# Kernel tuning notes

Measured on AMD Instinct MI355X. Metric: run time of the kernel, lower is better.

The kernel has to match this reference:

```python
import jax, jax.numpy as jnp
import numpy as np
from jax import lax

DIM = 384
NE = 8
TOPK = 2
HID = 4 * DIM
N, H, W = 32, 32, 32
EPS = 1e-6


def setup_inputs() -> dict:
    key = jax.random.key(0)
    ks = jax.random.split(key, 12)
    s = 0.02
    return {
        "input": jax.random.normal(ks[0], (N, DIM, H, W), dtype=jnp.float32),
        "dw_w": jax.random.normal(ks[1], (DIM, 1, 7, 7), dtype=jnp.float32) * s,
        "dw_b": jnp.zeros((DIM,), dtype=jnp.float32),
        "ln_g": jnp.ones((DIM,), dtype=jnp.float32),
        "ln_b": jnp.zeros((DIM,), dtype=jnp.float32),
        "gate_w": jax.random.normal(ks[2], (NE, DIM), dtype=jnp.float32) * s,
        "w1": jax.random.normal(ks[3], (NE, DIM, HID), dtype=jnp.float32) * s,
        "b1": jnp.zeros((NE, HID), dtype=jnp.float32),
        "w2": jax.random.normal(ks[4], (NE, HID, DIM), dtype=jnp.float32) * s,
        "b2": jnp.zeros((NE, DIM), dtype=jnp.float32),
        "layer_scale": jnp.ones((DIM, 1, 1), dtype=jnp.float32) * 1e-6,
    }


def reference(input, dw_w, dw_b, ln_g, ln_b, gate_w, w1, b1, w2, b2, layer_scale):
    # depthwise 7x7 conv, padding 3, groups=DIM  (NCHW)
    x = lax.conv_general_dilated(
        input, dw_w, window_strides=(1, 1), padding=((3, 3), (3, 3)),
        dimension_numbers=("NCHW", "OIHW", "NCHW"), feature_group_count=DIM,
    ) + dw_b[None, :, None, None]
    # permute to NHWC, layernorm over C with eps=1e-6
    x = jnp.transpose(x, (0, 2, 3, 1))
    mu = jnp.mean(x, axis=-1, keepdims=True)
    var = jnp.mean(jnp.square(x - mu), axis=-1, keepdims=True)
    x = (x - mu) * lax.rsqrt(var + EPS) * ln_g + ln_b

    x_flat = x.reshape(-1, DIM)  # [T, C]
    logits = x_flat @ gate_w.T   # [T, NE]
    topv, topi = lax.top_k(logits, TOPK)
    weights = jax.nn.softmax(topv, axis=-1)  # [T, K]

    # combine: out[t] = sum_e gate_e[t] * Expert_e(x_flat[t]), gate nonzero only for top-k
    out = jnp.zeros_like(x_flat)
    for e in range(NE):
        we = jnp.sum(jnp.where(topi == e, weights, 0.0), axis=-1)  # [T]
        h = jax.nn.gelu(x_flat @ w1[e] + b1[e], approximate=False)
        y = h @ w2[e] + b2[e]
        out = out + y * we[:, None]

    out = out.reshape(N, H, W, DIM)
    out = jnp.transpose(out, (0, 3, 1, 2))  # back to NCHW
    out = layer_scale[None] * out           # [C,1,1] broadcast
    # stochastic_depth prob 0.0 -> identity
    return input + out
```

## Files before the change

### kernel.cpp

```cpp
#include <hip/hip_runtime.h>
#include <hip/hip_bf16.h>

typedef __attribute__((ext_vector_type(4))) float  f32x4;
typedef __attribute__((ext_vector_type(8))) short  s16x8;
typedef __attribute__((ext_vector_type(8))) unsigned short u16x8;
typedef __attribute__((ext_vector_type(4))) unsigned short u16x4;

#define DIM 384
#define NE 8
#define HID 1536
#define NB 32
#define HW 1024
#define T_TOK 32768

__device__ __forceinline__ unsigned short f2bf(float f) {
    unsigned int u = __float_as_uint(f);
    u = (u + 0x7fffu + ((u >> 16) & 1u)) >> 16;
    return (unsigned short)u;
}
__device__ __forceinline__ float bf2f(unsigned short u) {
    return __uint_as_float((unsigned int)u << 16);
}

__global__ __launch_bounds__(256) void k_transpose(const float* __restrict__ src,
                                                   unsigned short* __restrict__ dst,
                                                   int R, int C) {
    int b = blockIdx.x;
    int ctiles = C >> 5;
    int rtiles = R >> 5;
    int ct = b % ctiles;
    int rt = (b / ctiles) % rtiles;
    int e  = b / (ctiles * rtiles);
    __shared__ float t[32][33];
    int tid = threadIdx.x;
    const float* s = src + (size_t)e * R * C;
    unsigned short* d = dst + (size_t)e * C * R;
#pragma unroll
    for (int k = 0; k < 4; ++k) {
        int idx = k * 256 + tid;
        int rr = idx >> 5, cc = idx & 31;
        t[rr][cc] = s[(size_t)(rt * 32 + rr) * C + ct * 32 + cc];
    }
    __syncthreads();
#pragma unroll
    for (int k = 0; k < 4; ++k) {
        int idx = k * 256 + tid;
        int cc = idx >> 5, rr = idx & 31;
        d[(size_t)(ct * 32 + cc) * R + rt * 32 + rr] = f2bf(t[rr][cc]);
    }
}

__global__ __launch_bounds__(256) void k_conv(const float* __restrict__ in,
                                              const float* __restrict__ dw_w,
                                              const float* __restrict__ dw_b,
                                              float* __restrict__ xconv) {
    int nc = blockIdx.x;
    int c = nc % DIM;
    __shared__ float tile[38 * 38];
    __shared__ float wt[49];
    const float* plane = in + (size_t)nc * HW;
    int tid = threadIdx.x;
    if (tid < 49) wt[tid] = dw_w[c * 49 + tid];
    for (int idx = tid; idx < 38 * 38; idx += 256) {
        int ty = idx / 38, tx = idx % 38;
        int ih = ty - 3, iw = tx - 3;
        float v = 0.f;
        if ((unsigned)ih < 32u && (unsigned)iw < 32u) v = plane[ih * 32 + iw];
        tile[idx] = v;
    }
    __syncthreads();
    float bias = dw_b[c];
    int w = tid & 31, h0 = (tid >> 5) << 2;
    float acc[4] = {bias, bias, bias, bias};
#pragma unroll
    for (int iy = 0; iy < 10; ++iy) {
        float r[7];
#pragma unroll
        for (int dx = 0; dx < 7; ++dx) r[dx] = tile[(h0 + iy) * 38 + w + dx];
#pragma unroll
        for (int o = 0; o < 4; ++o) {
            int dy = iy - o;
            if (dy >= 0 && dy < 7) {
                float a = 0.f;
#pragma unroll
                for (int dx = 0; dx < 7; ++dx) a += r[dx] * wt[dy * 7 + dx];
                acc[o] += a;
            }
        }
    }
    float* outp = xconv + (size_t)nc * HW;
#pragma unroll
    for (int o = 0; o < 4; ++o) outp[(h0 + o) * 32 + w] = acc[o];
}

__global__ __launch_bounds__(256) void k_ln_gate(const float* __restrict__ xconv,
                                                 const float* __restrict__ ln_g,
                                                 const float* __restrict__ ln_b,
                                                 const float* __restrict__ gate_w,
                                                 unsigned short* __restrict__ lnout,
                                                 int* __restrict__ lists,
                                                 float* __restrict__ wgts,
                                                 int* __restrict__ counts) {
    __shared__ float xs[32][385];
    __shared__ float gw[8][384];
    __shared__ float gls[384], bls[384];
    __shared__ int hcnt[8], hbase[8];
    __shared__ int lexp[32][2];
    __shared__ int lpos[32][2];
    __shared__ float lw[32][2];

    int b = blockIdx.x;
    int n = b >> 5;
    int hw0 = (b & 31) << 5;
    int tid = threadIdx.x;

    for (int i = tid; i < 384; i += 256) { gls[i] = ln_g[i]; bls[i] = ln_b[i]; }
    for (int i = tid; i < 8 * 384; i += 256) gw[i / 384][i % 384] = gate_w[i];
    if (tid < 8) hcnt[tid] = 0;

    const float* base = xconv + (size_t)n * DIM * HW + hw0;
#pragma unroll
    for (int k = 0; k < 48; ++k) {
        int idx = k * 256 + tid;
        int c = idx >> 5, j = idx & 31;
        xs[j][c] = base[(size_t)c * HW + j];
    }
    __syncthreads();

    int tok = tid >> 3, jj = tid & 7;
    float sum = 0.f, sq = 0.f;
#pragma unroll
    for (int k = 0; k < 48; ++k) {
        float v = xs[tok][jj + 8 * k];
        sum += v; sq += v * v;
    }
#pragma unroll
    for (int m = 1; m < 8; m <<= 1) { sum += __shfl_xor(sum, m); sq += __shfl_xor(sq, m); }
    float mu = sum * (1.f / 384.f);
    float var = sq * (1.f / 384.f) - mu * mu;
    float rstd = rsqrtf(var + 1e-6f);

    int tglob = n * HW + hw0 + tok;
    float p[8] = {0, 0, 0, 0, 0, 0, 0, 0};
#pragma unroll
    for (int k = 0; k < 48; ++k) {
        int c = jj + 8 * k;
        float v = (xs[tok][c] - mu) * rstd * gls[c] + bls[c];
        lnout[(size_t)tglob * DIM + c] = f2bf(v);
#pragma unroll
        for (int e = 0; e < 8; ++e) p[e] += v * gw[e][c];
    }
#pragma unroll
    for (int e = 0; e < 8; ++e)
#pragma unroll
        for (int m = 1; m < 8; m <<= 1) p[e] += __shfl_xor(p[e], m);

    if (jj == 0) {
        int i0 = 0; float v0 = p[0];
#pragma unroll
        for (int e = 1; e < 8; ++e) if (p[e] > v0) { v0 = p[e]; i0 = e; }
        int i1 = -1; float v1 = -1e30f;
#pragma unroll
        for (int e = 0; e < 8; ++e) if (e != i0 && p[e] > v1) { v1 = p[e]; i1 = e; }
        float w0 = 1.f / (1.f + __expf(v1 - v0));
        float w1 = 1.f - w0;
        lexp[tok][0] = i0; lexp[tok][1] = i1;
        lw[tok][0] = w0;  lw[tok][1] = w1;
        lpos[tok][0] = atomicAdd(&hcnt[i0], 1);
        lpos[tok][1] = atomicAdd(&hcnt[i1], 1);
    }
    __syncthreads();
    if (tid < 8) hbase[tid] = atomicAdd(&counts[tid], hcnt[tid]);
    __syncthreads();
    if (jj == 0) {
#pragma unroll
        for (int s = 0; s < 2; ++s) {
            int e = lexp[tok][s];
            int pos = hbase[e] + lpos[tok][s];
            lists[e * T_TOK + pos] = (tglob << 1) | s;
            wgts[e * T_TOK + pos] = lw[tok][s];
        }
    }
}

__global__ __launch_bounds__(512, 2) void k_moe(const unsigned short* __restrict__ ln,
                                                const unsigned short* __restrict__ w1t,
                                                const unsigned short* __restrict__ w2t,
                                                const float* __restrict__ b1,
                                                const float* __restrict__ b2,
                                                const int* __restrict__ lists,
                                                const float* __restrict__ wgts,
                                                const int* __restrict__ counts,
                                                unsigned short* __restrict__ y0,
                                                unsigned short* __restrict__ y1) {
    int e    = blockIdx.x & 7;
    int tile = blockIdx.x >> 3;
    int cnt = counts[e];
    if (tile * 128 >= cnt) return;

    __shared__ unsigned short X[128][392];
    __shared__ unsigned short Hs[128][136];
    __shared__ int   ents[128];
    __shared__ float wrow[128];

    int tid = threadIdx.x;
    if (tid < 128) {
        int idx = tile * 128 + tid;
        if (idx < cnt) { ents[tid] = lists[e * T_TOK + idx]; wrow[tid] = wgts[e * T_TOK + idx]; }
        else           { ents[tid] = -1;                     wrow[tid] = 0.f; }
    }
    __syncthreads();

    {
        int row = tid >> 2, q = tid & 3;
        int ent = ents[row];
        int tok = (ent < 0) ? 0 : (ent >> 1);
        const u16x8* src = (const u16x8*)(ln + (size_t)tok * DIM);
        u16x8* dst = (u16x8*)(&X[row][0]);
#pragma unroll
        for (int r = 0; r < 12; ++r) dst[q + r * 4] = __builtin_nontemporal_load(&src[q + r * 4]);
    }
    __syncthreads();

    int wid = tid >> 6;
    int lane = tid & 63;
    int lr = lane & 15;
    int lq = lane >> 4;

    const s16x8* q1 = (const s16x8*)(w1t + ((size_t)e * HID + wid * 16 + lr) * DIM + lq * 8);
    const s16x8* q2 = (const s16x8*)(w2t + ((size_t)e * DIM + wid * 48 + lr) * HID + lq * 8);

    f32x4 Yacc[3][8] = {};

    for (int hc = 0; hc < 12; ++hc) {
        const s16x8* q1h = q1 + hc * 6144;
        s16x8 wall[12];
#pragma unroll
        for (int k = 0; k < 12; ++k) wall[k] = q1h[k * 4];
        f32x4 bv = *(const f32x4*)&b1[e * HID + hc * 128 + wid * 16 + lq * 4];
        f32x4 Hf[8];
#pragma unroll
        for (int m = 0; m < 8; ++m) Hf[m] = bv;
        __builtin_amdgcn_s_setprio(1);
#pragma unroll
        for (int k = 0; k < 12; ++k) {
#pragma unroll
            for (int m = 0; m < 8; ++m) {
                s16x8 a = *(const s16x8*)&X[m * 16 + lr][k * 32 + lq * 8];
                Hf[m] = __builtin_amdgcn_mfma_f32_16x16x32_bf16(wall[k], a, Hf[m], 0, 0, 0);
            }
        }
        __builtin_amdgcn_s_setprio(0);
        s16x8 vall[12];
#pragma unroll
        for (int t = 0; t < 12; ++t) {
            int nj = t % 3, k2 = t / 3;
            vall[t] = q2[nj * 3072 + hc * 16 + k2 * 4];
        }
#pragma unroll
        for (int m = 0; m < 8; ++m) {
            u16x4 pk;
#pragma unroll
            for (int r = 0; r < 4; ++r) {
                float v = Hf[m][r];
                float t = v * fmaf(v * v, -0.07135481627f, -1.5957691216f);
                float g = v * __builtin_amdgcn_rcpf(1.f + __expf(t));
                pk[r] = f2bf(g);
            }
            *(u16x4*)&Hs[m * 16 + lr][wid * 16 + lq * 4] = pk;
        }
        asm volatile("s_waitcnt lgkmcnt(0)" ::: "memory");
        __builtin_amdgcn_s_barrier();
        __builtin_amdgcn_sched_barrier(0);
        __builtin_amdgcn_s_setprio(1);
#pragma unroll
        for (int k2 = 0; k2 < 4; ++k2) {
#pragma unroll
            for (int m = 0; m < 8; ++m) {
                s16x8 a = *(const s16x8*)&Hs[m * 16 + lr][k2 * 32 + lq * 8];
#pragma unroll
                for (int nj = 0; nj < 3; ++nj) {
                    Yacc[nj][m] = __builtin_amdgcn_mfma_f32_16x16x32_bf16(vall[k2 * 3 + nj], a, Yacc[nj][m], 0, 0, 0);
                }
            }
        }
        __builtin_amdgcn_s_setprio(0);
        asm volatile("s_waitcnt lgkmcnt(0)" ::: "memory");
        __builtin_amdgcn_s_barrier();
        __builtin_amdgcn_sched_barrier(0);
    }

    f32x4 b2v[3];
#pragma unroll
    for (int nj = 0; nj < 3; ++nj)
        b2v[nj] = *(const f32x4*)&b2[e * DIM + wid * 48 + nj * 16 + lq * 4];
#pragma unroll
    for (int m = 0; m < 8; ++m) {
        int row = m * 16 + lr;
        int ent = ents[row];
        if (ent >= 0) {
            float wv = wrow[row];
            int tok = ent >> 1;
            unsigned short* yb = (ent & 1) ? y1 : y0;
#pragma unroll
            for (int nj = 0; nj < 3; ++nj) {
                u16x4 pk;
#pragma unroll
                for (int r = 0; r < 4; ++r)
                    pk[r] = f2bf((Yacc[nj][m][r] + b2v[nj][r]) * wv);
                *(u16x4*)(yb + (size_t)tok * DIM + wid * 48 + nj * 16 + lq * 4) = pk;
            }
        }
    }
}

__global__ __launch_bounds__(256) void k_final(const float* __restrict__ input,
                                               const float* __restrict__ ls,
                                               const unsigned short* __restrict__ y0,
                                               const unsigned short* __restrict__ y1,
                                               float* __restrict__ out) {
    int b = blockIdx.x;
    int ct = b % 12;
    int hwt = (b / 12) % 32;
    int n = b / (12 * 32);
    int c0 = ct * 32, hw0 = hwt * 32;
    __shared__ float t[32][33];
    int tid = threadIdx.x;
    int t0 = n * HW + hw0;
#pragma unroll
    for (int k = 0; k < 2; ++k) {
        int idx = k * 256 + tid;
        int tl = idx >> 4, pr = idx & 15;
        size_t o = (size_t)(t0 + tl) * DIM + c0 + pr * 2;
        unsigned int a = *(const unsigned int*)(y0 + o);
        unsigned int c = *(const unsigned int*)(y1 + o);
        t[tl][pr * 2]     = bf2f((unsigned short)a) + bf2f((unsigned short)c);
        t[tl][pr * 2 + 1] = bf2f((unsigned short)(a >> 16)) + bf2f((unsigned short)(c >> 16));
    }
    __syncthreads();
#pragma unroll
    for (int k = 0; k < 4; ++k) {
        int idx = k * 256 + tid;
        int cl = idx >> 5, j = idx & 31;
        size_t o = ((size_t)n * DIM + c0 + cl) * HW + hw0 + j;
        out[o] = input[o] + ls[c0 + cl] * t[j][cl];
    }
}

extern "C" void kernel_launch(void* const* d_in, const int* in_sizes, int n_in,
                              void* d_out, int out_size, void* d_ws, size_t ws_size,
                              hipStream_t stream) {
    const float* input  = (const float*)d_in[0];
    const float* dw_w   = (const float*)d_in[1];
    const float* dw_b   = (const float*)d_in[2];
    const float* ln_g   = (const float*)d_in[3];
    const float* ln_b   = (const float*)d_in[4];
    const float* gate_w = (const float*)d_in[5];
    const float* w1     = (const float*)d_in[6];
    const float* b1     = (const float*)d_in[7];
    const float* w2     = (const float*)d_in[8];
    const float* b2     = (const float*)d_in[9];
    const float* lscale = (const float*)d_in[10];

    const size_t SZ_PLANE = (size_t)NB * DIM * HW * 4;
    const size_t SZ_YBF   = (size_t)T_TOK * DIM * 2;
    char* ws = (char*)d_ws;
    float* xconv = (float*)(ws + 0);
    unsigned short* y0 = (unsigned short*)(ws + 0);
    unsigned short* y1 = (unsigned short*)(ws + SZ_YBF);
    unsigned short* lnb = (unsigned short*)(ws + SZ_PLANE);
    unsigned short* w1t = (unsigned short*)(ws + SZ_PLANE + 25165824);
    unsigned short* w2t = (unsigned short*)(ws + SZ_PLANE + 25165824 + 9437184);
    int*   lists  = (int*)(ws + SZ_PLANE + 25165824 + 2 * 9437184);
    float* wgt    = (float*)(ws + SZ_PLANE + 25165824 + 2 * 9437184 + 1048576);
    int*   counts = (int*)(ws + SZ_PLANE + 25165824 + 2 * 9437184 + 2 * 1048576);
    const size_t needed = SZ_PLANE + 25165824 + 2 * 9437184 + 2 * 1048576 + 256;
    if (ws_size < needed) return;

    hipMemsetAsync(counts, 0, 32, stream);
    k_transpose<<<8 * 12 * 48, 256, 0, stream>>>(w1, w1t, DIM, HID);
    k_transpose<<<8 * 48 * 12, 256, 0, stream>>>(w2, w2t, HID, DIM);
    k_conv<<<NB * DIM, 256, 0, stream>>>(input, dw_w, dw_b, xconv);
    k_ln_gate<<<T_TOK / 32, 256, 0, stream>>>(xconv, ln_g, ln_b, gate_w, lnb, lists, wgt, counts);
    k_moe<<<NE * 256, 512, 0, stream>>>(lnb, w1t, w2t, b1, b2, lists, wgt, counts, y0, y1);
    k_final<<<NB * 32 * 12, 256, 0, stream>>>(input, lscale, y0, y1, (float*)d_out);
}
```

Baseline: 427.6 us.

## Switch MoE expert GEMMs and activations from bf16 to fp8 e4m3

Weights, layernorm output and the GELU hidden activations are now stored as fp8 e4m3 rather than bf16, and both expert matmuls use the fp8 16x16x32 MFMA. The aim is to halve global and LDS traffic for weights and tokens. The next hidden chunk's w1 fragment is now loaded after the first GEMM so it overlaps the GELU and second GEMM, and w2 loads are issued earlier. The instruction shape keeps K=32, so MFMA issue count is unchanged. It also costs noticeably more quantization error, which is masked only by the tiny layer_scale.

```diff
diff --git a/kernel.cpp b/kernel.cpp
--- a/kernel.cpp
+++ b/kernel.cpp
@@ -1,10 +1,11 @@
 #include <hip/hip_runtime.h>
 #include <hip/hip_bf16.h>
+#include <hip/hip_fp8.h>
 
 typedef __attribute__((ext_vector_type(4))) float  f32x4;
-typedef __attribute__((ext_vector_type(8))) short  s16x8;
 typedef __attribute__((ext_vector_type(8))) unsigned short u16x8;
 typedef __attribute__((ext_vector_type(4))) unsigned short u16x4;
+typedef long long f8x8;
 
 #define DIM 384
 #define NE 8
@@ -21,10 +22,14 @@
 __device__ __forceinline__ float bf2f(unsigned short u) {
     return __uint_as_float((unsigned int)u << 16);
 }
-
-__global__ __launch_bounds__(256) void k_transpose(const float* __restrict__ src,
-                                                   unsigned short* __restrict__ dst,
-                                                   int R, int C) {
+__device__ __forceinline__ unsigned char f2fp8(float f) {
+    __hip_fp8_e4m3 h(f);
+    return (unsigned char)h.__x;
+}
+
+__global__ __launch_bounds__(256) void k_transpose8(const float* __restrict__ src,
+                                                    unsigned char* __restrict__ dst,
+                                                    int R, int C) {
     int b = blockIdx.x;
     int ctiles = C >> 5;
     int rtiles = R >> 5;
@@ -34,7 +39,7 @@
     __shared__ float t[32][33];
     int tid = threadIdx.x;
     const float* s = src + (size_t)e * R * C;
-    unsigned short* d = dst + (size_t)e * C * R;
+    unsigned char* d = dst + (size_t)e * C * R;
 #pragma unroll
     for (int k = 0; k < 4; ++k) {
         int idx = k * 256 + tid;
@@ -42,12 +47,12 @@
         t[rr][cc] = s[(size_t)(rt * 32 + rr) * C + ct * 32 + cc];
     }
     __syncthreads();
-#pragma unroll
-    for (int k = 0; k < 4; ++k) {
-        int idx = k * 256 + tid;
-        int cc = idx >> 5, rr = idx & 31;
-        d[(size_t)(ct * 32 + cc) * R + rt * 32 + rr] = f2bf(t[rr][cc]);
-    }
+    int cc = tid >> 3, r4 = tid & 7;
+    unsigned int pk = 0;
+#pragma unroll
+    for (int i = 0; i < 4; ++i)
+        pk |= (unsigned int)f2fp8(t[r4 * 4 + i][cc]) << (8 * i);
+    *(unsigned int*)&d[(size_t)(ct * 32 + cc) * R + rt * 32 + r4 * 4] = pk;
 }
 
 __global__ __launch_bounds__(256) void k_conv(const float* __restrict__ in,
@@ -97,7 +102,7 @@
                                                  const float* __restrict__ ln_g,
                                                  const float* __restrict__ ln_b,
                                                  const float* __restrict__ gate_w,
-                                                 unsigned short* __restrict__ lnout,
+                                                 unsigned char* __restrict__ lnout,
                                                  int* __restrict__ lists,
                                                  float* __restrict__ wgts,
                                                  int* __restrict__ counts) {
@@ -146,7 +151,7 @@
     for (int k = 0; k < 48; ++k) {
         int c = jj + 8 * k;
         float v = (xs[tok][c] - mu) * rstd * gls[c] + bls[c];
-        lnout[(size_t)tglob * DIM + c] = f2bf(v);
+        lnout[(size_t)tglob * DIM + c] = f2fp8(v);
 #pragma unroll
         for (int e = 0; e < 8; ++e) p[e] += v * gw[e][c];
     }
@@ -183,9 +188,9 @@
     }
 }
 
-__global__ __launch_bounds__(512, 2) void k_moe(const unsigned short* __restrict__ ln,
-                                                const unsigned short* __restrict__ w1t,
-                                                const unsigned short* __restrict__ w2t,
+__global__ __launch_bounds__(512, 2) void k_moe(const unsigned char* __restrict__ ln,
+                                                const unsigned char* __restrict__ w1t,
+                                                const unsigned char* __restrict__ w2t,
                                                 const float* __restrict__ b1,
                                                 const float* __restrict__ b2,
                                                 const int* __restrict__ lists,
@@ -198,8 +203,8 @@
     int cnt = counts[e];
     if (tile * 128 >= cnt) return;
 
-    __shared__ unsigned short X[128][392];
-    __shared__ unsigned short Hs[128][136];
+    __shared__ unsigned char X[128][400];
+    __shared__ unsigned char Hs[128][136];
     __shared__ int   ents[128];
     __shared__ float wrow[128];
 
@@ -216,9 +221,9 @@
         int ent = ents[row];
         int tok = (ent < 0) ? 0 : (ent >> 1);
         const u16x8* src = (const u16x8*)(ln + (size_t)tok * DIM);
-        u16x8* dst = (u16x8*)(&X[row][0]);
-#pragma unroll
-        for (int r = 0; r < 12; ++r) dst[q + r * 4] = __builtin_nontemporal_load(&src[q + r * 4]);
+#pragma unroll
+        for (int r = 0; r < 6; ++r)
+            *(u16x8*)&X[row][(q + r * 4) * 16] = __builtin_nontemporal_load(&src[q + r * 4]);
     }
     __syncthreads();
 
@@ -227,16 +232,22 @@
     int lr = lane & 15;
     int lq = lane >> 4;
 
-    const s16x8* q1 = (const s16x8*)(w1t + ((size_t)e * HID + wid * 16 + lr) * DIM + lq * 8);
-    const s16x8* q2 = (const s16x8*)(w2t + ((size_t)e * DIM + wid * 48 + lr) * HID + lq * 8);
+    const unsigned char* pw1 = w1t + ((size_t)e * HID + wid * 16 + lr) * DIM + lq * 8;
+    const unsigned char* pw2 = w2t + ((size_t)e * DIM + wid * 48 + lr) * HID + lq * 8;
 
     f32x4 Yacc[3][8] = {};
 
+    f8x8 wall[12];
+#pragma unroll
+    for (int k = 0; k < 12; ++k) wall[k] = *(const f8x8*)(pw1 + k * 32);
+
     for (int hc = 0; hc < 12; ++hc) {
-        const s16x8* q1h = q1 + hc * 6144;
-        s16x8 wall[12];
-#pragma unroll
-        for (int k = 0; k < 12; ++k) wall[k] = q1h[k * 4];
+        f8x8 vall[12];
+#pragma unroll
+        for (int t = 0; t < 12; ++t) {
+            int nj = t % 3, k2 = t / 3;
+            vall[t] = *(const f8x8*)(pw2 + (size_t)nj * 16 * HID + hc * 128 + k2 * 32);
+        }
         f32x4 bv = *(const f32x4*)&b1[e * HID + hc * 128 + wid * 16 + lq * 4];
         f32x4 Hf[8];
 #pragma unroll
@@ -246,28 +257,27 @@
         for (int k = 0; k < 12; ++k) {
 #pragma unroll
             for (int m = 0; m < 8; ++m) {
-                s16x8 a = *(const s16x8*)&X[m * 16 + lr][k * 32 + lq * 8];
-                Hf[m] = __builtin_amdgcn_mfma_f32_16x16x32_bf16(wall[k], a, Hf[m], 0, 0, 0);
+                f8x8 a = *(const f8x8*)&X[m * 16 + lr][k * 32 + lq * 8];
+                Hf[m] = __builtin_amdgcn_mfma_f32_16x16x32_fp8_fp8(wall[k], a, Hf[m], 0, 0, 0);
             }
         }
         __builtin_amdgcn_s_setprio(0);
-        s16x8 vall[12];
-#pragma unroll
-        for (int t = 0; t < 12; ++t) {
-            int nj = t % 3, k2 = t / 3;
-            vall[t] = q2[nj * 3072 + hc * 16 + k2 * 4];
+        if (hc < 11) {
+            const unsigned char* pn = pw1 + (size_t)(hc + 1) * 128 * DIM;
+#pragma unroll
+            for (int k = 0; k < 12; ++k) wall[k] = *(const f8x8*)(pn + k * 32);
         }
 #pragma unroll
         for (int m = 0; m < 8; ++m) {
-            u16x4 pk;
+            unsigned int pk = 0;
 #pragma unroll
             for (int r = 0; r < 4; ++r) {
                 float v = Hf[m][r];
                 float t = v * fmaf(v * v, -0.07135481627f, -1.5957691216f);
                 float g = v * __builtin_amdgcn_rcpf(1.f + __expf(t));
-                pk[r] = f2bf(g);
-            }
-            *(u16x4*)&Hs[m * 16 + lr][wid * 16 + lq * 4] = pk;
+                pk |= (unsigned int)f2fp8(g) << (8 * r);
+            }
+            *(unsigned int*)&Hs[m * 16 + lr][wid * 16 + lq * 4] = pk;
         }
         asm volatile("s_waitcnt lgkmcnt(0)" ::: "memory");
         __builtin_amdgcn_s_barrier();
@@ -277,10 +287,10 @@
         for (int k2 = 0; k2 < 4; ++k2) {
 #pragma unroll
             for (int m = 0; m < 8; ++m) {
-                s16x8 a = *(const s16x8*)&Hs[m * 16 + lr][k2 * 32 + lq * 8];
+                f8x8 h = *(const f8x8*)&Hs[m * 16 + lr][k2 * 32 + lq * 8];
 #pragma unroll
                 for (int nj = 0; nj < 3; ++nj) {
-                    Yacc[nj][m] = __builtin_amdgcn_mfma_f32_16x16x32_bf16(vall[k2 * 3 + nj], a, Yacc[nj][m], 0, 0, 0);
+                    Yacc[nj][m] = __builtin_amdgcn_mfma_f32_16x16x32_fp8_fp8(vall[k2 * 3 + nj], h, Yacc[nj][m], 0, 0, 0);
                 }
             }
         }
@@ -364,22 +374,24 @@
 
     const size_t SZ_PLANE = (size_t)NB * DIM * HW * 4;
     const size_t SZ_YBF   = (size_t)T_TOK * DIM * 2;
+    const size_t SZ_LNB   = (size_t)T_TOK * DIM;
+    const size_t SZ_W1    = (size_t)NE * DIM * HID;
     char* ws = (char*)d_ws;
     float* xconv = (float*)(ws + 0);
     unsigned short* y0 = (unsigned short*)(ws + 0);
     unsigned short* y1 = (unsigned short*)(ws + SZ_YBF);
-    unsigned short* lnb = (unsigned short*)(ws + SZ_PLANE);
-    unsigned short* w1t = (unsigned short*)(ws + SZ_PLANE + 25165824);
-    unsigned short* w2t = (unsigned short*)(ws + SZ_PLANE + 25165824 + 9437184);
-    int*   lists  = (int*)(ws + SZ_PLANE + 25165824 + 2 * 9437184);
-    float* wgt    = (float*)(ws + SZ_PLANE + 25165824 + 2 * 9437184 + 1048576);
-    int*   counts = (int*)(ws + SZ_PLANE + 25165824 + 2 * 9437184 + 2 * 1048576);
-    const size_t needed = SZ_PLANE + 25165824 + 2 * 9437184 + 2 * 1048576 + 256;
+    unsigned char* lnb = (unsigned char*)(ws + SZ_PLANE);
+    unsigned char* w1t = (unsigned char*)(ws + SZ_PLANE + SZ_LNB);
+    unsigned char* w2t = (unsigned char*)(ws + SZ_PLANE + SZ_LNB + SZ_W1);
+    int*   lists  = (int*)(ws + SZ_PLANE + SZ_LNB + 2 * SZ_W1);
+    float* wgt    = (float*)(ws + SZ_PLANE + SZ_LNB + 2 * SZ_W1 + 1048576);
+    int*   counts = (int*)(ws + SZ_PLANE + SZ_LNB + 2 * SZ_W1 + 2 * 1048576);
+    const size_t needed = SZ_PLANE + SZ_LNB + 2 * SZ_W1 + 2 * 1048576 + 256;
     if (ws_size < needed) return;
 
     hipMemsetAsync(counts, 0, 32, stream);
-    k_transpose<<<8 * 12 * 48, 256, 0, stream>>>(w1, w1t, DIM, HID);
-    k_transpose<<<8 * 48 * 12, 256, 0, stream>>>(w2, w2t, HID, DIM);
+    k_transpose8<<<8 * 12 * 48, 256, 0, stream>>>(w1, w1t, DIM, HID);
+    k_transpose8<<<8 * 48 * 12, 256, 0, stream>>>(w2, w2t, HID, DIM);
     k_conv<<<NB * DIM, 256, 0, stream>>>(input, dw_w, dw_b, xconv);
     k_ln_gate<<<T_TOK / 32, 256, 0, stream>>>(xconv, ln_g, ln_b, gate_w, lnb, lists, wgt, counts);
     k_moe<<<NE * 256, 512, 0, stream>>>(lnb, w1t, w2t, b1, b2, lists, wgt, counts, y0, y1);
```

Measured after the change: 407.7 us. 1.05x faster.
